# Kernel optimization log

Measured on AMD Instinct MI355X. Metric: run time of the kernel, lower is better.

## Reference

```python
import jax, jax.numpy as jnp
import numpy as np

B, T, C = 2, 2048, 1024
E, K = 8, 2            # n_experts, top_k (n_experts_active)
H = 2736               # round8(int(4*C*2/3)) SwiGLU hidden dim


def setup_inputs() -> dict:
    key = jax.random.key(0)
    ks = jax.random.split(key, 8)
    def w(k, shape, fan_in):
        return jax.random.normal(k, shape, jnp.float32) * (1.0 / np.sqrt(fan_in))
    x = jax.random.normal(ks[0], (B, T, C), jnp.float32)
    router_w = w(ks[1], (C, E), C)          # gate.weight.T
    wg = w(ks[2], (E, C, H), C)             # stacked expert w_gate.weight.T
    wu = w(ks[3], (E, C, H), C)             # stacked expert w_up.weight.T
    wd = w(ks[4], (E, H, C), H)             # stacked expert w_down.weight.T
    sg = w(ks[5], (C, H), C)                # shared expert gate
    su = w(ks[6], (C, H), C)                # shared expert up
    sd = w(ks[7], (H, C), H)                # shared expert down
    return {"x": x, "router_w": router_w, "wg": wg, "wu": wu, "wd": wd,
            "sg": sg, "su": su, "sd": sd}


def reference(x, router_w, wg, wu, wd, sg, su, sd):
    Bx, Tx, Cx = x.shape
    xf = x.reshape(-1, Cx)                       # (Tk, C)
    Tk = xf.shape[0]

    # --- router ---
    logits = xf @ router_w                       # (Tk, E)
    top_v, top_i = jax.lax.top_k(logits, K)      # (Tk, K)
    rw = jax.nn.softmax(top_v, axis=-1)          # normalized weights over selected

    # combine weights per (token, expert): scatter router weights
    rows = jnp.arange(Tk)[:, None]
    w_te = jnp.zeros((Tk, E), xf.dtype).at[rows, top_i].add(rw)   # (Tk, E)

    # --- experts (dense dispatch; weight w_te zeros out unselected experts) ---
    gate = jnp.einsum('tc,ech->teh', xf, wg)     # (Tk, E, H)
    up = jnp.einsum('tc,ech->teh', xf, wu)
    h = jax.nn.silu(gate) * up                   # SwiGLU hidden
    out = jnp.einsum('teh,te,ehc->tc', h, w_te, wd)   # weighted combine

    # --- shared expert ---
    out = out + (jax.nn.silu(xf @ sg) * (xf @ su)) @ sd

    # --- aux load-balancing loss ---
    mask = jnp.zeros((Tk, E), xf.dtype).at[rows, top_i].add(1.0)
    f = mask.mean(axis=0) / K
    p = jax.nn.softmax(logits, axis=-1).mean(axis=0)
    aux_loss = E * (f * p).sum()

    return out.reshape(Bx, Tx, Cx), aux_loss
```

## Files before the change

kernel.cpp:

```cpp
#include <hip/hip_runtime.h>

typedef _Float16 f16;
typedef _Float16 f16x4 __attribute__((ext_vector_type(4)));
typedef _Float16 f16x8 __attribute__((ext_vector_type(8)));
typedef float f32x4 __attribute__((ext_vector_type(4)));

#define TK 4096
#define CD 1024
#define HD 2736
#define HP 2816
#define MT 104
#define RC 13312

#define GLDS16(ldsp, gp) __builtin_amdgcn_global_load_lds( \
    (const __attribute__((address_space(1))) unsigned int*)(gp), \
    (__attribute__((address_space(3))) unsigned int*)(ldsp), 16, 0, 0)

static constexpr size_t WS_XB  = 0;
static constexpr size_t WS_H   = WS_XB  + (size_t)TK*CD*2;
static constexpr size_t WS_WGT = WS_H   + (size_t)RC*HP*2;
static constexpr size_t WS_WUT = WS_WGT + (size_t)8*HP*CD*2;
static constexpr size_t WS_WDT = WS_WUT + (size_t)8*HP*CD*2;
static constexpr size_t WS_SGT = WS_WDT + (size_t)8*CD*HP*2;
static constexpr size_t WS_SUT = WS_SGT + (size_t)HP*CD*2;
static constexpr size_t WS_SDT = WS_SUT + (size_t)HP*CD*2;
static constexpr size_t WS_CT  = WS_SDT + (size_t)CD*HP*2;
static constexpr size_t CT_STOK = 0;
static constexpr size_t CT_SW   = CT_STOK + (size_t)RC*4;
static constexpr size_t CT_TI   = CT_SW   + (size_t)RC*4;
static constexpr size_t CT_TW   = CT_TI   + (size_t)TK*2*4;
static constexpr size_t CT_ISL  = CT_TW   + (size_t)TK*2*4;
static constexpr size_t CT_CNT  = CT_ISL  + (size_t)TK*2*4;
static constexpr size_t CT_PS   = CT_CNT  + 32;
static constexpr size_t CT_CUR  = CT_PS   + 32;
static constexpr size_t CT_OFF  = CT_CUR  + 32;
static constexpr size_t CT_SIZE = CT_OFF  + 64;

__device__ __forceinline__ void tr_body(const float* __restrict__ src,
                                        f16* __restrict__ dst,
                                        int R, int Cc, int Rp) {
    const int tid = threadIdx.x;
    const int l = tid & 63, w = tid >> 6;
    const int cc0 = blockIdx.x * 128 + w * 32 + (l >> 3) * 4;
    const int rr0 = blockIdx.y * 64 + (l & 7) * 8;
    float4 v[8];
    #pragma unroll
    for (int e = 0; e < 8; e++) {
        int gr = rr0 + e;
        if (gr < R && cc0 + 3 < Cc) {
            v[e] = *(const float4*)(src + (size_t)gr * Cc + cc0);
        } else {
            float* ve = (float*)&v[e];
            #pragma unroll
            for (int c = 0; c < 4; c++)
                ve[c] = (gr < R && cc0 + c < Cc) ? src[(size_t)gr * Cc + cc0 + c] : 0.f;
        }
    }
    #pragma unroll
    for (int c = 0; c < 4; c++) {
        const float* vp = (const float*)v;
        f16x8 o = { (f16)vp[0*4+c], (f16)vp[1*4+c], (f16)vp[2*4+c], (f16)vp[3*4+c],
                    (f16)vp[4*4+c], (f16)vp[5*4+c], (f16)vp[6*4+c], (f16)vp[7*4+c] };
        *(f16x8*)(dst + (size_t)(cc0 + c) * Rp + rr0) = o;
    }
}

__global__ __launch_bounds__(256) void k_tr2(
    const float* __restrict__ wg, f16* __restrict__ wgt,
    const float* __restrict__ sg, f16* __restrict__ sgt,
    const float* __restrict__ wu, f16* __restrict__ wut,
    const float* __restrict__ su, f16* __restrict__ sut,
    int R, int Cc, int Rp, size_t sstride, size_t dstride) {
    const int z = blockIdx.z;
    const float* src; f16* dst;
    if (z < 9) {
        if (z < 8) { src = wg + (size_t)z * sstride; dst = wgt + (size_t)z * dstride; }
        else       { src = sg; dst = sgt; }
    } else {
        int z2 = z - 9;
        if (z2 < 8) { src = wu + (size_t)z2 * sstride; dst = wut + (size_t)z2 * dstride; }
        else        { src = su; dst = sut; }
    }
    tr_body(src, dst, R, Cc, Rp);
}

__global__ __launch_bounds__(256) void k_tr(
    const float* __restrict__ srcMain, f16* __restrict__ dstMain,
    const float* __restrict__ srcSh,   f16* __restrict__ dstSh,
    int R, int Cc, int Rp, int nMain, size_t sstride, size_t dstride) {
    const float* src; f16* dst;
    if ((int)blockIdx.z < nMain) {
        src = srcMain + (size_t)blockIdx.z * sstride;
        dst = dstMain + (size_t)blockIdx.z * dstride;
    } else {
        src = srcSh; dst = dstSh;
    }
    tr_body(src, dst, R, Cc, Rp);
}

__global__ void k_router(const float* __restrict__ x, const float* __restrict__ rw,
                         f16* __restrict__ xb,
                         int* __restrict__ topi, float* __restrict__ topw,
                         int* __restrict__ cnt, float* __restrict__ psum) {
    __shared__ float pl[8];
    int tid = threadIdx.x;
    if (tid < 8) pl[tid] = 0.f;
    __syncthreads();
    int wave = tid >> 6, lane = tid & 63;
    int t = blockIdx.x * 4 + wave;
    float acc[8];
    #pragma unroll
    for (int e = 0; e < 8; e++) acc[e] = 0.f;
    const float* xr = x + (size_t)t * CD;
    f16* xbr = xb + (size_t)t * CD;
    for (int i = 0; i < CD / 64; i++) {
        int c = lane + i * 64;
        float xv = xr[c];
        xbr[c] = (f16)xv;
        const float* wr = rw + c * 8;
        #pragma unroll
        for (int e = 0; e < 8; e++) acc[e] = fmaf(xv, wr[e], acc[e]);
    }
    #pragma unroll
    for (int e = 0; e < 8; e++) {
        #pragma unroll
        for (int off = 32; off; off >>= 1) acc[e] += __shfl_xor(acc[e], off);
    }
    if (lane == 0) {
        float v1 = -1e30f; int i1 = 0;
        #pragma unroll
        for (int e = 0; e < 8; e++) if (acc[e] > v1) { v1 = acc[e]; i1 = e; }
        float v2 = -1e30f; int i2 = (i1 == 0) ? 1 : 0;
        #pragma unroll
        for (int e = 0; e < 8; e++) if (e != i1 && acc[e] > v2) { v2 = acc[e]; i2 = e; }
        float b = expf(v2 - v1);
        float w1 = 1.f / (1.f + b);
        topi[t*2] = i1; topi[t*2+1] = i2;
        topw[t*2] = w1; topw[t*2+1] = b * w1;
        atomicAdd(&cnt[i1], 1);
        atomicAdd(&cnt[i2], 1);
        float m = acc[0];
        #pragma unroll
        for (int e = 1; e < 8; e++) m = fmaxf(m, acc[e]);
        float pe[8]; float s = 0.f;
        #pragma unroll
        for (int e = 0; e < 8; e++) { pe[e] = expf(acc[e] - m); s += pe[e]; }
        float inv = 1.f / s;
        #pragma unroll
        for (int e = 0; e < 8; e++) atomicAdd(&pl[e], pe[e] * inv);
    }
    __syncthreads();
    if (tid < 8) atomicAdd(&psum[tid], pl[tid]);
}

__global__ void k_prefix(const int* __restrict__ cnt, int* __restrict__ cur,
                         int* __restrict__ offs) {
    if (threadIdx.x == 0 && blockIdx.x == 0) {
        int off = 0;
        for (int e = 0; e < 8; e++) {
            offs[e] = off; cur[e] = off;
            off += (cnt[e] + 127) & ~127;
        }
        offs[8] = off;
        offs[9] = RC;
    }
}

__global__ void k_scatter(const int* __restrict__ topi, const float* __restrict__ topw,
                          int* __restrict__ cur, const int* __restrict__ offs,
                          int* __restrict__ stok, float* __restrict__ sw) {
    int t = blockIdx.x * 256 + threadIdx.x;
    if (t >= TK) return;
    #pragma unroll
    for (int s = 0; s < 2; s++) {
        int e = topi[t*2 + s];
        int pos = atomicAdd(&cur[e], 1);
        stok[pos] = t;
        sw[pos] = topw[t*2 + s];
    }
    int base = offs[8];
    stok[base + t] = t;
    sw[base + t] = 1.0f;
}

__global__ __launch_bounds__(256, 3) void k_ffn1(
    const f16* __restrict__ xb, const f16* __restrict__ wgt,
    const f16* __restrict__ wut, const f16* __restrict__ sgt,
    const f16* __restrict__ sut, const int* __restrict__ offs,
    const int* __restrict__ cnt, const int* __restrict__ stok,
    f16* __restrict__ hbuf)
{
    __shared__ f16 As[128*64];
    __shared__ f16 Bg[128*64];
    __shared__ f16 Bu[128*64];

    const int flat = blockIdx.y * gridDim.x + blockIdx.x;
    const int nwg  = gridDim.x * gridDim.y;
    const int wgid = (flat & 7) * (nwg >> 3) + (flat >> 3);
    const int n0 = (wgid % gridDim.x) * 128;
    const int m0 = (wgid / gridDim.x) * 128;

    int g = 0;
    while (g < 8 && m0 >= offs[g+1]) g++;
    if (m0 >= offs[8] + TK) return;
    if (g < 8 && (m0 - offs[g]) >= cnt[g]) return;

    const f16* __restrict__ Wg = (g < 8) ? wgt + (size_t)g * HP * CD : sgt;
    const f16* __restrict__ Wu = (g < 8) ? wut + (size_t)g * HP * CD : sut;

    const int tid = threadIdx.x;
    const int lane = tid & 63;
    const int w = tid >> 6;
    const int w32 = w * 32;

    const int asw = (((lane & 7) ^ (lane >> 3)) << 3);
    int rA[4];
    #pragma unroll
    for (int i = 0; i < 4; i++)
        rA[i] = stok[m0 + w32 + 8*i + (lane >> 3)] * CD + asw;
    const int rB = (n0 + w32 + (lane >> 3)) * CD + asw;

    f32x4 accg[4][4], accu[4][4];
    #pragma unroll
    for (int i = 0; i < 4; i++)
        #pragma unroll
        for (int j = 0; j < 4; j++)
            #pragma unroll
            for (int r = 0; r < 4; r++) { accg[i][j][r] = 0.f; accu[i][j][r] = 0.f; }

    const int wm = (w >> 1) * 64;
    const int wn = (w & 1) * 64;
    const int fm = lane & 15;
    const int fq = lane >> 4;
    const int fs = fm & 7;

    for (int k0 = 0; k0 < CD; k0 += 64) {
        #pragma unroll
        for (int i = 0; i < 4; i++) {
            GLDS16(&As[(w32 + 8*i) * 64], xb + rA[i] + k0);
            GLDS16(&Bg[(w32 + 8*i) * 64], Wg + rB + i*8*CD + k0);
            GLDS16(&Bu[(w32 + 8*i) * 64], Wu + rB + i*8*CD + k0);
        }
        __syncthreads();
        #pragma unroll
        for (int kk = 0; kk < 2; kk++) {
            const int sw = ((((kk << 2) | fq) ^ fs) << 3);
            f16x8 af[4];
            #pragma unroll
            for (int mi = 0; mi < 4; mi++)
                af[mi] = *(const f16x8*)&As[(wm + mi*16 + fm) * 64 + sw];
            #pragma unroll
            for (int ni = 0; ni < 4; ni++) {
                f16x8 bgf = *(const f16x8*)&Bg[(wn + ni*16 + fm) * 64 + sw];
                f16x8 bur = *(const f16x8*)&Bu[(wn + ni*16 + fm) * 64 + sw];
                #pragma unroll
                for (int mi = 0; mi < 4; mi++) {
                    accg[mi][ni] = __builtin_amdgcn_mfma_f32_16x16x32_f16(af[mi], bgf, accg[mi][ni], 0, 0, 0);
                    accu[mi][ni] = __builtin_amdgcn_mfma_f32_16x16x32_f16(af[mi], bur, accu[mi][ni], 0, 0, 0);
                }
            }
        }
        __syncthreads();
    }

    #pragma unroll
    for (int mi = 0; mi < 4; mi++) {
        #pragma unroll
        for (int ni = 0; ni < 4; ni++) {
            #pragma unroll
            for (int r = 0; r < 4; r++) {
                int row = m0 + wm + mi*16 + fq*4 + r;
                int col = n0 + wn + ni*16 + fm;
                float gv = accg[mi][ni][r];
                float uv = accu[mi][ni][r];
                float hv = gv / (1.f + __expf(-gv)) * uv;
                hbuf[(size_t)row * HP + col] = (f16)hv;
            }
        }
    }
}

__global__ __launch_bounds__(256, 4) void k_ffn2(
    const f16* __restrict__ hbuf, const f16* __restrict__ wdt,
    const f16* __restrict__ sdt, const int* __restrict__ offs,
    const int* __restrict__ cnt, const int* __restrict__ stok,
    const float* __restrict__ swt, float* __restrict__ out)
{
    __shared__ f16 As[128*64];
    __shared__ f16 Bs[128*64];

    const int flat = blockIdx.y * gridDim.x + blockIdx.x;
    const int nwg  = gridDim.x * gridDim.y;
    const int wgid = (flat & 7) * (nwg >> 3) + (flat >> 3);
    const int n0 = (wgid % gridDim.x) * 128;
    const int m0 = (wgid / gridDim.x) * 128;

    int g = 0;
    while (g < 8 && m0 >= offs[g+1]) g++;
    if (m0 >= offs[8] + TK) return;
    if (g < 8 && (m0 - offs[g]) >= cnt[g]) return;
    const f16* __restrict__ W = (g < 8) ? wdt + (size_t)g * CD * HP : sdt;

    const int tid = threadIdx.x;
    const int lane = tid & 63;
    const int w = tid >> 6;
    const int w32 = w * 32;

    const int asw = (((lane & 7) ^ (lane >> 3)) << 3);
    const int rA = (m0 + w32 + (lane >> 3)) * HP + asw;
    const int rB = (n0 + w32 + (lane >> 3)) * HP + asw;

    f32x4 acc[4][4];
    #pragma unroll
    for (int i = 0; i < 4; i++)
        #pragma unroll
        for (int j = 0; j < 4; j++)
            #pragma unroll
            for (int r = 0; r < 4; r++) acc[i][j][r] = 0.f;

    const int wm = (w >> 1) * 64;
    const int wn = (w & 1) * 64;
    const int fm = lane & 15;
    const int fq = lane >> 4;
    const int fs = fm & 7;

    for (int k0 = 0; k0 < HP; k0 += 64) {
        #pragma unroll
        for (int i = 0; i < 4; i++) {
            GLDS16(&As[(w32 + 8*i) * 64], hbuf + (size_t)rA + i*8*HP + k0);
            GLDS16(&Bs[(w32 + 8*i) * 64], W    + (size_t)rB + i*8*HP + k0);
        }
        __syncthreads();
        #pragma unroll
        for (int kk = 0; kk < 2; kk++) {
            const int sw = ((((kk << 2) | fq) ^ fs) << 3);
            f16x8 af[4];
            #pragma unroll
            for (int mi = 0; mi < 4; mi++)
                af[mi] = *(const f16x8*)&As[(wm + mi*16 + fm) * 64 + sw];
            #pragma unroll
            for (int ni = 0; ni < 4; ni++) {
                f16x8 bfr = *(const f16x8*)&Bs[(wn + ni*16 + fm) * 64 + sw];
                #pragma unroll
                for (int mi = 0; mi < 4; mi++)
                    acc[mi][ni] = __builtin_amdgcn_mfma_f32_16x16x32_f16(af[mi], bfr, acc[mi][ni], 0, 0, 0);
            }
        }
        __syncthreads();
    }

    #pragma unroll
    for (int mi = 0; mi < 4; mi++) {
        #pragma unroll
        for (int r = 0; r < 4; r++) {
            int row = m0 + wm + mi*16 + fq*4 + r;
            int t = stok[row];
            float rowW = swt[row];
            float* orow = out + (size_t)t * CD + n0;
            #pragma unroll
            for (int ni = 0; ni < 4; ni++) {
                int col = wn + ni*16 + fm;
                atomicAdd(orow + col, rowW * acc[mi][ni][r]);
            }
        }
    }
}

__global__ void k_aux(const int* __restrict__ cnt, const float* __restrict__ psum,
                      float* __restrict__ out_aux) {
    if (threadIdx.x == 0 && blockIdx.x == 0) {
        float a = 0.f;
        for (int e = 0; e < 8; e++) {
            float f = (float)cnt[e] / ((float)TK * 2.f);
            float p = psum[e] / (float)TK;
            a += f * p;
        }
        out_aux[0] = 8.f * a;
    }
}

extern "C" void kernel_launch(void* const* d_in, const int* in_sizes, int n_in,
                              void* d_out, int out_size, void* d_ws, size_t ws_size,
                              hipStream_t stream) {
    const float* x  = (const float*)d_in[0];
    const float* rw = (const float*)d_in[1];
    const float* wg = (const float*)d_in[2];
    const float* wu = (const float*)d_in[3];
    const float* wd = (const float*)d_in[4];
    const float* sg = (const float*)d_in[5];
    const float* su = (const float*)d_in[6];
    const float* sd = (const float*)d_in[7];
    float* out = (float*)d_out;

    char* ws = (char*)d_ws;
    f16* xb   = (f16*)(ws + WS_XB);
    f16* hbuf = (f16*)(ws + WS_H);
    f16* wgt  = (f16*)(ws + WS_WGT);
    f16* wut  = (f16*)(ws + WS_WUT);
    f16* wdt  = (f16*)(ws + WS_WDT);
    f16* sgt  = (f16*)(ws + WS_SGT);
    f16* sut  = (f16*)(ws + WS_SUT);
    f16* sdt  = (f16*)(ws + WS_SDT);
    char* ct  = ws + WS_CT;
    int*   stok = (int*)  (ct + CT_STOK);
    float* swt  = (float*)(ct + CT_SW);
    int*   topi = (int*)  (ct + CT_TI);
    float* topw = (float*)(ct + CT_TW);
    int*   cnt  = (int*)  (ct + CT_CNT);
    float* psum = (float*)(ct + CT_PS);
    int*   cur  = (int*)  (ct + CT_CUR);
    int*   offs = (int*)  (ct + CT_OFF);

    hipMemsetAsync(ct, 0, CT_SIZE, stream);
    hipMemsetAsync(out, 0, (size_t)TK * CD * 4, stream);

    k_router<<<dim3(TK / 4), dim3(256), 0, stream>>>(x, rw, xb, topi, topw, cnt, psum);
    k_prefix<<<dim3(1), dim3(64), 0, stream>>>(cnt, cur, offs);
    k_scatter<<<dim3(TK / 256), dim3(256), 0, stream>>>(topi, topw, cur, offs, stok, swt);

    k_tr2<<<dim3(HP/128, CD/64, 18), dim3(256), 0, stream>>>(
        wg, wgt, sg, sgt, wu, wut, su, sut, CD, HD, CD, (size_t)CD*HD, (size_t)HP*CD);
    k_tr<<<dim3(CD/128, HP/64, 9), dim3(256), 0, stream>>>(
        wd, wdt, sd, sdt, HD, CD, HP, 8, (size_t)HD*CD, (size_t)CD*HP);

    k_ffn1<<<dim3(HP/128, MT), dim3(256), 0, stream>>>(xb, wgt, wut, sgt, sut, offs, cnt, stok, hbuf);
    k_ffn2<<<dim3(CD/128, MT), dim3(256), 0, stream>>>(hbuf, wdt, sdt, offs, cnt, stok, swt, out);
    k_aux<<<dim3(1), dim3(64), 0, stream>>>(cnt, psum, out + (size_t)TK * CD);
}
```

Baseline: 785.0 us.

## Double-buffer FFN GEMM loads and replace atomic scatter with gather-combine

Both expert GEMM kernels now use a two-stage LDS ping-pong with a K step of 32. Explicit vmcnt waits, barriers and setprio are added so global-to-LDS copies overlap with MFMA work. The down-projection writes per-slot results to a scratch buffer that reuses the gate-weight workspace. A new combine kernel gathers the two expert rows and the shared row per token with router weights, which removes the float atomics and the output memset. The cost is extra memory traffic for the intermediate buffer and one more kernel launch.

```diff
diff --git a/kernel.cpp b/kernel.cpp
--- a/kernel.cpp
+++ b/kernel.cpp
@@ -25,6 +25,7 @@
 static constexpr size_t WS_SUT = WS_SGT + (size_t)HP*CD*2;
 static constexpr size_t WS_SDT = WS_SUT + (size_t)HP*CD*2;
 static constexpr size_t WS_CT  = WS_SDT + (size_t)CD*HP*2;
+static constexpr size_t WS_OBUF = WS_WGT;
 static constexpr size_t CT_STOK = 0;
 static constexpr size_t CT_SW   = CT_STOK + (size_t)RC*4;
 static constexpr size_t CT_TI   = CT_SW   + (size_t)RC*4;
@@ -168,7 +169,8 @@
 
 __global__ void k_scatter(const int* __restrict__ topi, const float* __restrict__ topw,
                           int* __restrict__ cur, const int* __restrict__ offs,
-                          int* __restrict__ stok, float* __restrict__ sw) {
+                          int* __restrict__ stok, float* __restrict__ sw,
+                          int* __restrict__ islot) {
     int t = blockIdx.x * 256 + threadIdx.x;
     if (t >= TK) return;
     #pragma unroll
@@ -177,6 +179,7 @@
         int pos = atomicAdd(&cur[e], 1);
         stok[pos] = t;
         sw[pos] = topw[t*2 + s];
+        islot[t*2 + s] = pos;
     }
     int base = offs[8];
     stok[base + t] = t;
@@ -190,9 +193,9 @@
     const int* __restrict__ cnt, const int* __restrict__ stok,
     f16* __restrict__ hbuf)
 {
-    __shared__ f16 As[128*64];
-    __shared__ f16 Bg[128*64];
-    __shared__ f16 Bu[128*64];
+    __shared__ f16 As[2][128*32];
+    __shared__ f16 Bg[2][128*32];
+    __shared__ f16 Bu[2][128*32];
 
     const int flat = blockIdx.y * gridDim.x + blockIdx.x;
     const int nwg  = gridDim.x * gridDim.y;
@@ -213,12 +216,14 @@
     const int w = tid >> 6;
     const int w32 = w * 32;
 
-    const int asw = (((lane & 7) ^ (lane >> 3)) << 3);
-    int rA[4];
-    #pragma unroll
-    for (int i = 0; i < 4; i++)
-        rA[i] = stok[m0 + w32 + 8*i + (lane >> 3)] * CD + asw;
-    const int rB = (n0 + w32 + (lane >> 3)) * CD + asw;
+    const int asw = (((lane & 3) ^ ((lane >> 3) & 3)) << 3);
+    const int lr  = lane >> 2;
+    int rA[2], rB[2];
+    #pragma unroll
+    for (int i = 0; i < 2; i++) {
+        rA[i] = stok[m0 + w32 + 16*i + lr] * CD + asw;
+        rB[i] = (n0 + w32 + 16*i + lr) * CD + asw;
+    }
 
     f32x4 accg[4][4], accu[4][4];
     #pragma unroll
@@ -232,36 +237,48 @@
     const int wn = (w & 1) * 64;
     const int fm = lane & 15;
     const int fq = lane >> 4;
-    const int fs = fm & 7;
-
-    for (int k0 = 0; k0 < CD; k0 += 64) {
-        #pragma unroll
-        for (int i = 0; i < 4; i++) {
-            GLDS16(&As[(w32 + 8*i) * 64], xb + rA[i] + k0);
-            GLDS16(&Bg[(w32 + 8*i) * 64], Wg + rB + i*8*CD + k0);
-            GLDS16(&Bu[(w32 + 8*i) * 64], Wu + rB + i*8*CD + k0);
-        }
-        __syncthreads();
-        #pragma unroll
-        for (int kk = 0; kk < 2; kk++) {
-            const int sw = ((((kk << 2) | fq) ^ fs) << 3);
-            f16x8 af[4];
-            #pragma unroll
-            for (int mi = 0; mi < 4; mi++)
-                af[mi] = *(const f16x8*)&As[(wm + mi*16 + fm) * 64 + sw];
-            #pragma unroll
-            for (int ni = 0; ni < 4; ni++) {
-                f16x8 bgf = *(const f16x8*)&Bg[(wn + ni*16 + fm) * 64 + sw];
-                f16x8 bur = *(const f16x8*)&Bu[(wn + ni*16 + fm) * 64 + sw];
-                #pragma unroll
-                for (int mi = 0; mi < 4; mi++) {
-                    accg[mi][ni] = __builtin_amdgcn_mfma_f32_16x16x32_f16(af[mi], bgf, accg[mi][ni], 0, 0, 0);
-                    accu[mi][ni] = __builtin_amdgcn_mfma_f32_16x16x32_f16(af[mi], bur, accu[mi][ni], 0, 0, 0);
-                }
-            }
-        }
-        __syncthreads();
-    }
+    const int swo = ((fq ^ ((fm >> 1) & 3)) << 3);
+
+#define FFN1_STAGE(B_, K_) do { \
+    _Pragma("unroll") \
+    for (int i_ = 0; i_ < 2; i_++) { \
+        GLDS16(&As[B_][(w32 + 16*i_)*32], xb + rA[i_] + (K_)); \
+        GLDS16(&Bg[B_][(w32 + 16*i_)*32], Wg + rB[i_] + (K_)); \
+        GLDS16(&Bu[B_][(w32 + 16*i_)*32], Wu + rB[i_] + (K_)); } } while (0)
+
+#define FFN1_COMP(B_) do { \
+    f16x8 af_[4]; \
+    _Pragma("unroll") \
+    for (int mi_ = 0; mi_ < 4; mi_++) \
+        af_[mi_] = *(const f16x8*)&As[B_][(wm + mi_*16 + fm)*32 + swo]; \
+    __builtin_amdgcn_s_setprio(1); \
+    _Pragma("unroll") \
+    for (int ni_ = 0; ni_ < 4; ni_++) { \
+        f16x8 bg_ = *(const f16x8*)&Bg[B_][(wn + ni_*16 + fm)*32 + swo]; \
+        f16x8 bu_ = *(const f16x8*)&Bu[B_][(wn + ni_*16 + fm)*32 + swo]; \
+        _Pragma("unroll") \
+        for (int mi_ = 0; mi_ < 4; mi_++) { \
+            accg[mi_][ni_] = __builtin_amdgcn_mfma_f32_16x16x32_f16(af_[mi_], bg_, accg[mi_][ni_], 0, 0, 0); \
+            accu[mi_][ni_] = __builtin_amdgcn_mfma_f32_16x16x32_f16(af_[mi_], bu_, accu[mi_][ni_], 0, 0, 0); } } \
+    __builtin_amdgcn_s_setprio(0); } while (0)
+
+    FFN1_STAGE(0, 0);
+    int cur = 0;
+    for (int k0 = 32; k0 < CD; k0 += 32) {
+        FFN1_STAGE(cur ^ 1, k0);
+        __builtin_amdgcn_sched_barrier(0);
+        asm volatile("s_waitcnt vmcnt(6)" ::: "memory");
+        __builtin_amdgcn_s_barrier();
+        __builtin_amdgcn_sched_barrier(0);
+        FFN1_COMP(cur);
+        __builtin_amdgcn_sched_barrier(0);
+        __builtin_amdgcn_s_barrier();
+        cur ^= 1;
+    }
+    asm volatile("s_waitcnt vmcnt(0)" ::: "memory");
+    __builtin_amdgcn_s_barrier();
+    __builtin_amdgcn_sched_barrier(0);
+    FFN1_COMP(cur);
 
     #pragma unroll
     for (int mi = 0; mi < 4; mi++) {
@@ -283,11 +300,10 @@
 __global__ __launch_bounds__(256, 4) void k_ffn2(
     const f16* __restrict__ hbuf, const f16* __restrict__ wdt,
     const f16* __restrict__ sdt, const int* __restrict__ offs,
-    const int* __restrict__ cnt, const int* __restrict__ stok,
-    const float* __restrict__ swt, float* __restrict__ out)
+    const int* __restrict__ cnt, float* __restrict__ obuf)
 {
-    __shared__ f16 As[128*64];
-    __shared__ f16 Bs[128*64];
+    __shared__ f16 As[2][128*32];
+    __shared__ f16 Bs[2][128*32];
 
     const int flat = blockIdx.y * gridDim.x + blockIdx.x;
     const int nwg  = gridDim.x * gridDim.y;
@@ -306,9 +322,14 @@
     const int w = tid >> 6;
     const int w32 = w * 32;
 
-    const int asw = (((lane & 7) ^ (lane >> 3)) << 3);
-    const int rA = (m0 + w32 + (lane >> 3)) * HP + asw;
-    const int rB = (n0 + w32 + (lane >> 3)) * HP + asw;
+    const int asw = (((lane & 3) ^ ((lane >> 3) & 3)) << 3);
+    const int lr  = lane >> 2;
+    size_t rA[2], rB[2];
+    #pragma unroll
+    for (int i = 0; i < 2; i++) {
+        rA[i] = (size_t)(m0 + w32 + 16*i + lr) * HP + asw;
+        rB[i] = (size_t)(n0 + w32 + 16*i + lr) * HP + asw;
+    }
 
     f32x4 acc[4][4];
     #pragma unroll
@@ -322,48 +343,79 @@
     const int wn = (w & 1) * 64;
     const int fm = lane & 15;
     const int fq = lane >> 4;
-    const int fs = fm & 7;
-
-    for (int k0 = 0; k0 < HP; k0 += 64) {
-        #pragma unroll
-        for (int i = 0; i < 4; i++) {
-            GLDS16(&As[(w32 + 8*i) * 64], hbuf + (size_t)rA + i*8*HP + k0);
-            GLDS16(&Bs[(w32 + 8*i) * 64], W    + (size_t)rB + i*8*HP + k0);
-        }
-        __syncthreads();
-        #pragma unroll
-        for (int kk = 0; kk < 2; kk++) {
-            const int sw = ((((kk << 2) | fq) ^ fs) << 3);
-            f16x8 af[4];
-            #pragma unroll
-            for (int mi = 0; mi < 4; mi++)
-                af[mi] = *(const f16x8*)&As[(wm + mi*16 + fm) * 64 + sw];
+    const int swo = ((fq ^ ((fm >> 1) & 3)) << 3);
+
+#define FFN2_STAGE(B_, K_) do { \
+    _Pragma("unroll") \
+    for (int i_ = 0; i_ < 2; i_++) { \
+        GLDS16(&As[B_][(w32 + 16*i_)*32], hbuf + rA[i_] + (K_)); \
+        GLDS16(&Bs[B_][(w32 + 16*i_)*32], W    + rB[i_] + (K_)); } } while (0)
+
+#define FFN2_COMP(B_) do { \
+    f16x8 af_[4]; \
+    _Pragma("unroll") \
+    for (int mi_ = 0; mi_ < 4; mi_++) \
+        af_[mi_] = *(const f16x8*)&As[B_][(wm + mi_*16 + fm)*32 + swo]; \
+    __builtin_amdgcn_s_setprio(1); \
+    _Pragma("unroll") \
+    for (int ni_ = 0; ni_ < 4; ni_++) { \
+        f16x8 bf_ = *(const f16x8*)&Bs[B_][(wn + ni_*16 + fm)*32 + swo]; \
+        _Pragma("unroll") \
+        for (int mi_ = 0; mi_ < 4; mi_++) \
+            acc[mi_][ni_] = __builtin_amdgcn_mfma_f32_16x16x32_f16(af_[mi_], bf_, acc[mi_][ni_], 0, 0, 0); } \
+    __builtin_amdgcn_s_setprio(0); } while (0)
+
+    FFN2_STAGE(0, 0);
+    int cur = 0;
+    for (int k0 = 32; k0 < HP; k0 += 32) {
+        FFN2_STAGE(cur ^ 1, k0);
+        __builtin_amdgcn_sched_barrier(0);
+        asm volatile("s_waitcnt vmcnt(4)" ::: "memory");
+        __builtin_amdgcn_s_barrier();
+        __builtin_amdgcn_sched_barrier(0);
+        FFN2_COMP(cur);
+        __builtin_amdgcn_sched_barrier(0);
+        __builtin_amdgcn_s_barrier();
+        cur ^= 1;
+    }
+    asm volatile("s_waitcnt vmcnt(0)" ::: "memory");
+    __builtin_amdgcn_s_barrier();
+    __builtin_amdgcn_sched_barrier(0);
+    FFN2_COMP(cur);
+
+    #pragma unroll
+    for (int mi = 0; mi < 4; mi++) {
+        #pragma unroll
+        for (int r = 0; r < 4; r++) {
+            int row = m0 + wm + mi*16 + fq*4 + r;
             #pragma unroll
             for (int ni = 0; ni < 4; ni++) {
-                f16x8 bfr = *(const f16x8*)&Bs[(wn + ni*16 + fm) * 64 + sw];
-                #pragma unroll
-                for (int mi = 0; mi < 4; mi++)
-                    acc[mi][ni] = __builtin_amdgcn_mfma_f32_16x16x32_f16(af[mi], bfr, acc[mi][ni], 0, 0, 0);
+                int col = n0 + wn + ni*16 + fm;
+                obuf[(size_t)row * CD + col] = acc[mi][ni][r];
             }
         }
-        __syncthreads();
-    }
-
-    #pragma unroll
-    for (int mi = 0; mi < 4; mi++) {
-        #pragma unroll
-        for (int r = 0; r < 4; r++) {
-            int row = m0 + wm + mi*16 + fq*4 + r;
-            int t = stok[row];
-            float rowW = swt[row];
-            float* orow = out + (size_t)t * CD + n0;
-            #pragma unroll
-            for (int ni = 0; ni < 4; ni++) {
-                int col = wn + ni*16 + fm;
-                atomicAdd(orow + col, rowW * acc[mi][ni][r]);
-            }
-        }
-    }
+    }
+}
+
+__global__ __launch_bounds__(256) void k_comb(
+    const float* __restrict__ obuf, const int* __restrict__ islot,
+    const float* __restrict__ topw, const int* __restrict__ offs,
+    float* __restrict__ out)
+{
+    const int t = blockIdx.x;
+    const int c = threadIdx.x * 4;
+    const int s0 = islot[t*2], s1 = islot[t*2+1];
+    const float w0 = topw[t*2], w1 = topw[t*2+1];
+    const int sh = offs[8] + t;
+    float4 a = *(const float4*)(obuf + (size_t)s0 * CD + c);
+    float4 b = *(const float4*)(obuf + (size_t)s1 * CD + c);
+    float4 s = *(const float4*)(obuf + (size_t)sh * CD + c);
+    float4 o;
+    o.x = fmaf(w0, a.x, fmaf(w1, b.x, s.x));
+    o.y = fmaf(w0, a.y, fmaf(w1, b.y, s.y));
+    o.z = fmaf(w0, a.z, fmaf(w1, b.z, s.z));
+    o.w = fmaf(w0, a.w, fmaf(w1, b.w, s.w));
+    *(float4*)(out + (size_t)t * CD + c) = o;
 }
 
 __global__ void k_aux(const int* __restrict__ cnt, const float* __restrict__ psum,
@@ -401,22 +453,23 @@
     f16* sgt  = (f16*)(ws + WS_SGT);
     f16* sut  = (f16*)(ws + WS_SUT);
     f16* sdt  = (f16*)(ws + WS_SDT);
+    float* obuf = (float*)(ws + WS_OBUF);
     char* ct  = ws + WS_CT;
     int*   stok = (int*)  (ct + CT_STOK);
     float* swt  = (float*)(ct + CT_SW);
     int*   topi = (int*)  (ct + CT_TI);
     float* topw = (float*)(ct + CT_TW);
+    int*   isl  = (int*)  (ct + CT_ISL);
     int*   cnt  = (int*)  (ct + CT_CNT);
     float* psum = (float*)(ct + CT_PS);
     int*   cur  = (int*)  (ct + CT_CUR);
     int*   offs = (int*)  (ct + CT_OFF);
 
     hipMemsetAsync(ct, 0, CT_SIZE, stream);
-    hipMemsetAsync(out, 0, (size_t)TK * CD * 4, stream);
 
     k_router<<<dim3(TK / 4), dim3(256), 0, stream>>>(x, rw, xb, topi, topw, cnt, psum);
     k_prefix<<<dim3(1), dim3(64), 0, stream>>>(cnt, cur, offs);
-    k_scatter<<<dim3(TK / 256), dim3(256), 0, stream>>>(topi, topw, cur, offs, stok, swt);
+    k_scatter<<<dim3(TK / 256), dim3(256), 0, stream>>>(topi, topw, cur, offs, stok, swt, isl);
 
     k_tr2<<<dim3(HP/128, CD/64, 18), dim3(256), 0, stream>>>(
         wg, wgt, sg, sgt, wu, wut, su, sut, CD, HD, CD, (size_t)CD*HD, (size_t)HP*CD);
@@ -424,6 +477,7 @@
         wd, wdt, sd, sdt, HD, CD, HP, 8, (size_t)HD*CD, (size_t)CD*HP);
 
     k_ffn1<<<dim3(HP/128, MT), dim3(256), 0, stream>>>(xb, wgt, wut, sgt, sut, offs, cnt, stok, hbuf);
-    k_ffn2<<<dim3(CD/128, MT), dim3(256), 0, stream>>>(hbuf, wdt, sdt, offs, cnt, stok, swt, out);
+    k_ffn2<<<dim3(CD/128, MT), dim3(256), 0, stream>>>(hbuf, wdt, sdt, offs, cnt, obuf);
+    k_comb<<<dim3(TK), dim3(256), 0, stream>>>(obuf, isl, topw, offs, out);
     k_aux<<<dim3(1), dim3(64), 0, stream>>>(cnt, psum, out + (size_t)TK * CD);
 }
```

Measured after the change: 778.6 us. About the same (-0.8%).
